# Kernel tuning notes

Hardware: AMD Instinct MI355X
Metric: run time of the kernel (lower is better)

## Reference

```python
import jax, jax.numpy as jnp
import numpy as np
from jax import lax

# module hyperparams (from init_kwargs)
K = 7
STRIDE = 1
PAD = 3
DIL = 1


def setup_inputs() -> dict:
    key = jax.random.key(0)
    ks = jax.random.split(key, 5)
    B, Cin, Cout, L = 4, 256, 256, 8192
    x = jax.random.normal(ks[0], (B, Cin, L), jnp.float32)
    # main conv weight (Cout, Cin, K), kaiming-ish scale
    weight = jax.random.normal(ks[1], (Cout, Cin, K), jnp.float32) * (1.0 / np.sqrt(Cin * K))
    bias = jax.random.normal(ks[2], (Cout,), jnp.float32) * 0.01
    # offset conv: Conv1d(Cin -> K, kernel K); small values so sampling is perturbed but in-range
    offset_w = jax.random.normal(ks[3], (K, Cin, K), jnp.float32) * 0.01
    offset_b = jax.random.normal(ks[4], (K,), jnp.float32) * 0.01
    return {"x": x, "weight": weight, "bias": bias, "offset_w": offset_w, "offset_b": offset_b}


def reference(x, weight, bias, offset_w, offset_b):
    B, Cin, L = x.shape
    out_len = (L + 2 * PAD - DIL * (K - 1) - 1) // STRIDE + 1

    # offset conv: (B, Cin, L) -> (B, K, out_len)
    offsets = lax.conv_general_dilated(
        x, offset_w, window_strides=(STRIDE,), padding=[(PAD, PAD)],
        rhs_dilation=(DIL,), dimension_numbers=("NCH", "OIH", "NCH"))
    offsets = offsets + offset_b[None, :, None]
    offsets = jnp.transpose(offsets, (0, 2, 1))  # (B, out_len, K)

    # standard sampling locations (1, out_len, K), shifted by padding as in original
    p = jnp.arange(out_len, dtype=jnp.float32)[None, :, None] * STRIDE
    p_k = (jnp.arange(K, dtype=jnp.float32) - (K - 1) / 2.0) * DIL
    loc = p + p_k[None, None, :] + PAD + offsets  # (B, out_len, K)

    # linear interpolation (clamped endpoints, matching torch clamp order)
    x0 = jnp.floor(loc).astype(jnp.int32)
    x1 = x0 + 1
    x0c = jnp.clip(x0, 0, L - 1)
    x1c = jnp.clip(x1, 0, L - 1)
    wa = x1c.astype(jnp.float32) - loc  # weights use clamped indices, as original
    wb = loc - x0c.astype(jnp.float32)

    # gather: per batch, (Cin, L)[:, (out_len, K)] -> (Cin, out_len, K)
    gather = jax.vmap(lambda xb, ib: xb[:, ib])
    fa = gather(x, x0c)  # (B, Cin, out_len, K)
    fb = gather(x, x1c)
    interp = wa[:, None] * fa + wb[:, None] * fb  # (B, Cin, out_len, K)

    # einsum 'blki,oik->blo' with interp laid out as (B, i=Cin, l, k)
    out = jnp.einsum("bilk,oik->bol", interp, weight) + bias[None, :, None]
    return out
```

## Files before the change

kernel.cpp:

```cpp
#include <hip/hip_runtime.h>
#include <hip/hip_bf16.h>


#define B_    4
#define CIN   256
#define COUT  256
#define LEN   8192
#define KK    7
#define NTOT  (B_ * LEN)
#define QTOT  (CIN * KK)
#define LPITCH 232

typedef short s16x8 __attribute__((ext_vector_type(8)));
typedef int   s32x4 __attribute__((ext_vector_type(4)));
typedef float f32x4 __attribute__((ext_vector_type(4)));

static __device__ __forceinline__ unsigned f2bf(float f) {
  union { float f; unsigned u; } u; u.f = f;
  unsigned r = u.u + 0x7FFF + ((u.u >> 16) & 1);
  return r >> 16;
}

static __device__ __forceinline__ int cvt_pk_bf16(float a, float b) {
  int r;
  asm("v_cvt_pk_bf16_f32 %0, %1, %2" : "=v"(r) : "v"(a), "v"(b));
  return r;
}

__global__ __launch_bounds__(256) void loc_partial(
    const float* __restrict__ X, const float* __restrict__ OW,
    float* __restrict__ Partial) {
  __shared__ float red[4][256][KK];

  const int t    = threadIdx.x;
  const int lane = t & 63;
  const int wu   = __builtin_amdgcn_readfirstlane(t >> 6);
  const int cg   = blockIdx.x >> 7;
  const int nb   = (blockIdx.x & 127) << 8;
  const int b    = nb >> 13;
  const int l0   = nb & (LEN - 1);

  float acc[KK][4];
#pragma unroll
  for (int k = 0; k < KK; ++k)
#pragma unroll
    for (int r = 0; r < 4; ++r) acc[k][r] = 0.0f;

#pragma unroll 2
  for (int ii = 0; ii < 16; ++ii) {
    const int i = cg * 64 + wu * 16 + ii;
    float owv[49];
#pragma unroll
    for (int k = 0; k < KK; ++k)
#pragma unroll
      for (int j = 0; j < KK; ++j)
        owv[k * 7 + j] = OW[(k * CIN + i) * KK + j];

    const float* xr = X + ((size_t)(b * CIN + i) << 13);
#pragma unroll
    for (int r = 0; r < 4; ++r) {
      const int lr = l0 + lane + 64 * r;
      float xv[KK];
#pragma unroll
      for (int j = 0; j < KK; ++j) {
        int pos = lr + j - 3;
        xv[j] = ((unsigned)pos < LEN) ? xr[pos] : 0.0f;
      }
#pragma unroll
      for (int k = 0; k < KK; ++k)
#pragma unroll
        for (int j = 0; j < KK; ++j)
          acc[k][r] += xv[j] * owv[k * 7 + j];
    }
  }

#pragma unroll
  for (int k = 0; k < KK; ++k)
#pragma unroll
    for (int r = 0; r < 4; ++r) red[wu][lane + 64 * r][k] = acc[k][r];
  __syncthreads();

#pragma unroll
  for (int k = 0; k < KK; ++k) {
    float s = red[0][t][k] + red[1][t][k] + red[2][t][k] + red[3][t][k];
    Partial[((size_t)(cg * 7 + k) << 15) + nb + t] = s;
  }
}

__global__ __launch_bounds__(256) void loc_reduce(
    const float* __restrict__ Partial, const float* __restrict__ OB,
    float* __restrict__ Loc) {
  int n = blockIdx.x * 256 + threadIdx.x;
  int l = n & (LEN - 1);
#pragma unroll
  for (int k = 0; k < KK; ++k) {
    float s = (float)(l + k) + OB[k];
#pragma unroll
    for (int cg = 0; cg < 4; ++cg)
      s += Partial[((size_t)(cg * 7 + k) << 15) + n];
    Loc[((size_t)k << 15) + n] = s;
  }
}

__global__ __launch_bounds__(256) void wt_build(
    const float* __restrict__ W, unsigned short* __restrict__ Wf) {
  __shared__ float Wl[16 * 32 * KK];
  const int t  = threadIdx.x;
  const int ot = blockIdx.x >> 3;
  const int c  = blockIdx.x & 7;

  for (int e = t; e < 16 * 32 * KK; e += 256) {
    int o = e / 224;
    int r = e - o * 224;
    Wl[e] = W[(size_t)(ot * 16 + o) * QTOT + c * 224 + r];
  }
  __syncthreads();

  const int lane = t & 63;
  const int sg   = t >> 6;
  const int ol   = lane & 15;
  const int ig   = lane >> 4;
  for (int s = sg; s < KK; s += 4) {
    s16x8 v;
#pragma unroll
    for (int j = 0; j < 8; ++j)
      v[j] = (short)f2bf(Wl[ol * 224 + (ig * 8 + j) * KK + s]);
    int f = (ot * 8 + c) * KK + s;
    *(s16x8*)(Wf + ((size_t)f << 9) + (lane << 3)) = v;
  }
}

__global__ __launch_bounds__(512, 4) void main_kernel(
    const float* __restrict__ X, const unsigned short* __restrict__ Wf,
    const float* __restrict__ Bias, const float* __restrict__ Loc,
    float* __restrict__ Out) {
  __shared__ unsigned short Il[2][64][LPITCH];

  const int t    = threadIdx.x;
  const int lane = t & 63;
  const int w    = t >> 6;
  const int n0   = blockIdx.x << 6;
  const int b    = n0 >> 13;
  const float* Xb = X + ((size_t)b << 21);

  const bool stager = (t < 448);
  const int nl = t & 63;
  const int kt = t >> 6;

  float c0 = 0.f, c1 = 0.f;
  const float* xp = Xb;
  if (stager) {
    float locv = Loc[((size_t)kt << 15) + n0 + nl];
    int x0  = (int)floorf(locv);
    int x0c = min(max(x0, 0), LEN - 1);
    int x1c = min(max(x0 + 1, 0), LEN - 1);
    float wa = (float)x1c - locv;
    float wb = locv - (float)x0c;
    bool hi = (x0 >= LEN - 1);
    bool lo = (x0 < 0);
    c0 = (hi ? 0.f : wa) + (lo ? wb : 0.f);
    c1 = (hi ? wa : 0.f) + (lo ? 0.f : wb);
    xp = Xb + min(max(x0, 0), LEN - 2);
  }

  f32x4 acc[2][4];
#pragma unroll
  for (int a = 0; a < 2; ++a)
#pragma unroll
    for (int cc = 0; cc < 4; ++cc) acc[a][cc] = (f32x4){0.f, 0.f, 0.f, 0.f};

  const int mrow = lane & 15;
  const int quad = lane >> 4;

  float f0[16], f1[16];

#define GATHER_H(chunk, h)                                        \
  if (stager) {                                                   \
    _Pragma("unroll")                                             \
    for (int m = 0; m < 16; ++m) {                                \
      const float* xr = xp + ((size_t)((chunk) * 32 + (h) * 16 + m) << 13); \
      f0[m] = xr[0];                                              \
      f1[m] = xr[1];                                              \
    }                                                             \
  }

#define CVT_H(dst, h)                                             \
  if (stager) {                                                   \
    s32x4 v0, v1;                                                 \
    _Pragma("unroll")                                             \
    for (int m = 0; m < 4; ++m) {                                 \
      float a = c0 * f0[2 * m]     + c1 * f1[2 * m];              \
      float d = c0 * f0[2 * m + 1] + c1 * f1[2 * m + 1];          \
      v0[m] = cvt_pk_bf16(a, d);                                  \
    }                                                             \
    _Pragma("unroll")                                             \
    for (int m = 0; m < 4; ++m) {                                 \
      float a = c0 * f0[8 + 2 * m]     + c1 * f1[8 + 2 * m];      \
      float d = c0 * f0[8 + 2 * m + 1] + c1 * f1[8 + 2 * m + 1];  \
      v1[m] = cvt_pk_bf16(a, d);                                  \
    }                                                             \
    *(s32x4*)((dst) + nl * LPITCH + kt * 32 + (h) * 16)     = v0; \
    *(s32x4*)((dst) + nl * LPITCH + kt * 32 + (h) * 16 + 8) = v1; \
  }

#define AFL(ttv, sv)                                              \
  (*(const s16x8*)(Wf + ((size_t)(((w * 2 + (ttv)) * 8 + c) * KK + (sv)) << 9) + (lane << 3)))

#define MSTEP(sv, a0, a1) {                                                        \
    const s16x8 b0 = *(const s16x8*)(Icur + (mrow)      * LPITCH + (sv) * 32 + quad * 8); \
    const s16x8 b1 = *(const s16x8*)(Icur + (16 + mrow) * LPITCH + (sv) * 32 + quad * 8); \
    acc[0][0] = __builtin_amdgcn_mfma_f32_16x16x32_bf16(a0, b0, acc[0][0], 0, 0, 0); \
    acc[1][0] = __builtin_amdgcn_mfma_f32_16x16x32_bf16(a1, b0, acc[1][0], 0, 0, 0); \
    acc[0][1] = __builtin_amdgcn_mfma_f32_16x16x32_bf16(a0, b1, acc[0][1], 0, 0, 0); \
    acc[1][1] = __builtin_amdgcn_mfma_f32_16x16x32_bf16(a1, b1, acc[1][1], 0, 0, 0); \
    const s16x8 b2 = *(const s16x8*)(Icur + (32 + mrow) * LPITCH + (sv) * 32 + quad * 8); \
    const s16x8 b3 = *(const s16x8*)(Icur + (48 + mrow) * LPITCH + (sv) * 32 + quad * 8); \
    acc[0][2] = __builtin_amdgcn_mfma_f32_16x16x32_bf16(a0, b2, acc[0][2], 0, 0, 0); \
    acc[1][2] = __builtin_amdgcn_mfma_f32_16x16x32_bf16(a1, b2, acc[1][2], 0, 0, 0); \
    acc[0][3] = __builtin_amdgcn_mfma_f32_16x16x32_bf16(a0, b3, acc[0][3], 0, 0, 0); \
    acc[1][3] = __builtin_amdgcn_mfma_f32_16x16x32_bf16(a1, b3, acc[1][3], 0, 0, 0); \
  }

  {
    unsigned short* I0 = &Il[0][0][0];
    GATHER_H(0, 0) CVT_H(I0, 0)
    GATHER_H(0, 1) CVT_H(I0, 1)
  }
  __syncthreads();

  for (int c = 0; c < 8; ++c) {
    const int cur = c & 1;
    const unsigned short* Icur = &Il[cur][0][0];
    unsigned short*       Inxt = &Il[cur ^ 1][0][0];

    s16x8 afA[2][4];
#pragma unroll
    for (int tt = 0; tt < 2; ++tt)
#pragma unroll
      for (int s = 0; s < 4; ++s) afA[tt][s] = AFL(tt, s);
    __builtin_amdgcn_sched_barrier(0);

    if (c < 7) { GATHER_H(c + 1, 0) }
    __builtin_amdgcn_sched_barrier(0);

    MSTEP(0, afA[0][0], afA[1][0])

    s16x8 afB[2][3];
#pragma unroll
    for (int tt = 0; tt < 2; ++tt)
#pragma unroll
      for (int s = 0; s < 3; ++s) afB[tt][s] = AFL(tt, 4 + s);
    __builtin_amdgcn_sched_barrier(0);

    MSTEP(1, afA[0][1], afA[1][1])

    if (c < 7) { CVT_H(Inxt, 0) GATHER_H(c + 1, 1) }
    __builtin_amdgcn_sched_barrier(0);

    MSTEP(2, afA[0][2], afA[1][2])
    MSTEP(3, afA[0][3], afA[1][3])
    MSTEP(4, afB[0][0], afB[1][0])

    if (c < 7) { CVT_H(Inxt, 1) }

    MSTEP(5, afB[0][1], afB[1][1])
    MSTEP(6, afB[0][2], afB[1][2])
    if (c < 7) __syncthreads();
  }
#undef GATHER_H
#undef CVT_H
#undef AFL
#undef MSTEP

  const int lbase = (n0 & (LEN - 1)) + mrow;
#pragma unroll
  for (int tt = 0; tt < 2; ++tt) {
    const int obase = (w * 2 + tt) * 16 + quad * 4;
#pragma unroll
    for (int r = 0; r < 4; ++r) {
      const int o = obase + r;
      const float bv = Bias[o];
      float* orow = Out + (((size_t)(b * COUT + o)) << 13) + lbase;
#pragma unroll
      for (int nt = 0; nt < 4; ++nt)
        orow[nt * 16] = acc[tt][nt][r] + bv;
    }
  }
}

extern "C" void kernel_launch(void* const* d_in, const int* in_sizes, int n_in,
                              void* d_out, int out_size, void* d_ws, size_t ws_size,
                              hipStream_t stream) {
  const float* X    = (const float*)d_in[0];
  const float* W    = (const float*)d_in[1];
  const float* Bias = (const float*)d_in[2];
  const float* OW   = (const float*)d_in[3];
  const float* OB   = (const float*)d_in[4];
  float* Out = (float*)d_out;

  float* Loc = (float*)d_ws;
  unsigned short* Wf = (unsigned short*)(Loc + (size_t)NTOT * KK);
  float* Partial = (float*)(Wf + (size_t)COUT * QTOT);

  loc_partial<<<4 * 128, 256, 0, stream>>>(X, OW, Partial);
  loc_reduce<<<NTOT / 256, 256, 0, stream>>>(Partial, OB, Loc);
  wt_build<<<128, 256, 0, stream>>>(W, Wf);
  main_kernel<<<NTOT / 64, 512, 0, stream>>>(X, Wf, Bias, Loc, Out);
}
```

Before: 184.7 us.

## Warp-specialize main kernel into MFMA waves and gather/stager waves

Splits the 8 waves of each block into 4 compute waves that each own 64 output channels (4x4 MFMA tiles) and 4 staging waves that gather, interpolate and convert X into the double-buffered LDS tile. Previously all waves interleaved gathering with MFMA under manual sched_barriers. The intent is to overlap global gather latency with matrix math through role separation and to simplify scheduling. In exchange, compute waves hold twice the accumulators and now load weight fragments inline instead of prefetching them. Half the waves do no MFMA, which may reduce matrix throughput or occupancy under the 512x4 launch bounds.

```diff
diff --git a/kernel.cpp b/kernel.cpp
--- a/kernel.cpp
+++ b/kernel.cpp
@@ -138,152 +138,165 @@
 
   const int t    = threadIdx.x;
   const int lane = t & 63;
-  const int w    = t >> 6;
+  const int w    = __builtin_amdgcn_readfirstlane(t >> 6);
   const int n0   = blockIdx.x << 6;
   const int b    = n0 >> 13;
   const float* Xb = X + ((size_t)b << 21);
 
-  const bool stager = (t < 448);
-  const int nl = t & 63;
-  const int kt = t >> 6;
-
-  float c0 = 0.f, c1 = 0.f;
-  const float* xp = Xb;
-  if (stager) {
-    float locv = Loc[((size_t)kt << 15) + n0 + nl];
-    int x0  = (int)floorf(locv);
-    int x0c = min(max(x0, 0), LEN - 1);
-    int x1c = min(max(x0 + 1, 0), LEN - 1);
-    float wa = (float)x1c - locv;
-    float wb = locv - (float)x0c;
-    bool hi = (x0 >= LEN - 1);
-    bool lo = (x0 < 0);
-    c0 = (hi ? 0.f : wa) + (lo ? wb : 0.f);
-    c1 = (hi ? wa : 0.f) + (lo ? 0.f : wb);
-    xp = Xb + min(max(x0, 0), LEN - 2);
-  }
-
-  f32x4 acc[2][4];
-#pragma unroll
-  for (int a = 0; a < 2; ++a)
-#pragma unroll
-    for (int cc = 0; cc < 4; ++cc) acc[a][cc] = (f32x4){0.f, 0.f, 0.f, 0.f};
-
   const int mrow = lane & 15;
   const int quad = lane >> 4;
-
-  float f0[16], f1[16];
-
-#define GATHER_H(chunk, h)                                        \
-  if (stager) {                                                   \
-    _Pragma("unroll")                                             \
-    for (int m = 0; m < 16; ++m) {                                \
-      const float* xr = xp + ((size_t)((chunk) * 32 + (h) * 16 + m) << 13); \
-      f0[m] = xr[0];                                              \
-      f1[m] = xr[1];                                              \
-    }                                                             \
-  }
-
-#define CVT_H(dst, h)                                             \
-  if (stager) {                                                   \
-    s32x4 v0, v1;                                                 \
-    _Pragma("unroll")                                             \
-    for (int m = 0; m < 4; ++m) {                                 \
-      float a = c0 * f0[2 * m]     + c1 * f1[2 * m];              \
-      float d = c0 * f0[2 * m + 1] + c1 * f1[2 * m + 1];          \
-      v0[m] = cvt_pk_bf16(a, d);                                  \
-    }                                                             \
-    _Pragma("unroll")                                             \
-    for (int m = 0; m < 4; ++m) {                                 \
-      float a = c0 * f0[8 + 2 * m]     + c1 * f1[8 + 2 * m];      \
-      float d = c0 * f0[8 + 2 * m + 1] + c1 * f1[8 + 2 * m + 1];  \
-      v1[m] = cvt_pk_bf16(a, d);                                  \
-    }                                                             \
-    *(s32x4*)((dst) + nl * LPITCH + kt * 32 + (h) * 16)     = v0; \
-    *(s32x4*)((dst) + nl * LPITCH + kt * 32 + (h) * 16 + 8) = v1; \
-  }
-
-#define AFL(ttv, sv)                                              \
-  (*(const s16x8*)(Wf + ((size_t)(((w * 2 + (ttv)) * 8 + c) * KK + (sv)) << 9) + (lane << 3)))
-
-#define MSTEP(sv, a0, a1) {                                                        \
-    const s16x8 b0 = *(const s16x8*)(Icur + (mrow)      * LPITCH + (sv) * 32 + quad * 8); \
-    const s16x8 b1 = *(const s16x8*)(Icur + (16 + mrow) * LPITCH + (sv) * 32 + quad * 8); \
+  const bool mf  = (w < 4);
+
+  const int sw   = w - 4;
+  const int nl   = lane;
+  const int ktA  = sw;
+  const int ktB  = sw + 4;
+  const bool hasB = (!mf) && (ktB < KK);
+
+  float c0A = 0.f, c1A = 0.f, c0B = 0.f, c1B = 0.f;
+  int offA = 0, offB = 0;
+  if (!mf) {
+    {
+      float locv = Loc[((size_t)ktA << 15) + n0 + nl];
+      int x0  = (int)floorf(locv);
+      int x0c = min(max(x0, 0), LEN - 1);
+      int x1c = min(max(x0 + 1, 0), LEN - 1);
+      float wa = (float)x1c - locv;
+      float wb = locv - (float)x0c;
+      bool hi = (x0 >= LEN - 1), lo = (x0 < 0);
+      c0A = (hi ? 0.f : wa) + (lo ? wb : 0.f);
+      c1A = (hi ? wa : 0.f) + (lo ? 0.f : wb);
+      offA = min(max(x0, 0), LEN - 2);
+    }
+    if (hasB) {
+      float locv = Loc[((size_t)ktB << 15) + n0 + nl];
+      int x0  = (int)floorf(locv);
+      int x0c = min(max(x0, 0), LEN - 1);
+      int x1c = min(max(x0 + 1, 0), LEN - 1);
+      float wa = (float)x1c - locv;
+      float wb = locv - (float)x0c;
+      bool hi = (x0 >= LEN - 1), lo = (x0 < 0);
+      c0B = (hi ? 0.f : wa) + (lo ? wb : 0.f);
+      c1B = (hi ? wa : 0.f) + (lo ? 0.f : wb);
+      offB = min(max(x0, 0), LEN - 2);
+    }
+  }
+
+  f32x4 acc[4][4];
+  if (mf) {
+#pragma unroll
+    for (int a = 0; a < 4; ++a)
+#pragma unroll
+      for (int cc = 0; cc < 4; ++cc) acc[a][cc] = (f32x4){0.f, 0.f, 0.f, 0.f};
+  }
+
+  float fX0[8], fX1[8], fY0[8], fY1[8];
+
+#define GQ(j, F0, F1) {                                               \
+    const int st_ = (j) >> 2; const int hh_ = (j) & 3;                \
+    if (st_ == 0 || hasB) {                                           \
+      const int o_ = st_ ? offBc : offAc;                             \
+      _Pragma("unroll")                                               \
+      for (int m = 0; m < 8; ++m) {                                   \
+        const int idx = o_ + ((hh_ * 8 + m) << 13);                   \
+        F0[m] = Xb[idx];                                              \
+        F1[m] = Xb[idx + 1];                                          \
+      }                                                               \
+    } }
+
+#define CQ(j, F0, F1, DST) {                                          \
+    const int st_ = (j) >> 2; const int hh_ = (j) & 3;                \
+    if (st_ == 0 || hasB) {                                           \
+      const float c0_ = st_ ? c0B : c0A;                              \
+      const float c1_ = st_ ? c1B : c1A;                              \
+      const int   kt_ = st_ ? ktB : ktA;                              \
+      s32x4 vv;                                                       \
+      _Pragma("unroll")                                               \
+      for (int m = 0; m < 4; ++m) {                                   \
+        float a = c0_ * F0[2 * m]     + c1_ * F1[2 * m];              \
+        float d = c0_ * F0[2 * m + 1] + c1_ * F1[2 * m + 1];          \
+        vv[m] = cvt_pk_bf16(a, d);                                    \
+      }                                                               \
+      *(s32x4*)((DST) + nl * LPITCH + kt_ * 32 + hh_ * 8) = vv;       \
+    } }
+
+#define STAGE(DST, CH0) {                                             \
+    const int offAc = offA + ((CH0) << 13);                           \
+    const int offBc = offB + ((CH0) << 13);                           \
+    GQ(0, fX0, fX1) GQ(1, fY0, fY1)                                   \
+    CQ(0, fX0, fX1, DST) GQ(2, fX0, fX1)                              \
+    CQ(1, fY0, fY1, DST) GQ(3, fY0, fY1)                              \
+    CQ(2, fX0, fX1, DST) GQ(4, fX0, fX1)                              \
+    CQ(3, fY0, fY1, DST) GQ(5, fY0, fY1)                              \
+    CQ(4, fX0, fX1, DST) GQ(6, fX0, fX1)                              \
+    CQ(5, fY0, fY1, DST) GQ(7, fY0, fY1)                              \
+    CQ(6, fX0, fX1, DST)                                              \
+    CQ(7, fY0, fY1, DST)                                              \
+  }
+
+#define AFL(ttv, sv)                                                  \
+  (*(const s16x8*)(Wf + ((size_t)(((w * 4 + (ttv)) * 8 + c) * KK + (sv)) << 9) + (lane << 3)))
+
+#define BLD(ro, sv)                                                   \
+  (*(const s16x8*)(Icur + ((ro) + mrow) * LPITCH + (sv) * 32 + quad * 8))
+
+#define MSTEP4(sv) {                                                  \
+    const s16x8 a0 = AFL(0, sv), a1 = AFL(1, sv);                     \
+    const s16x8 a2 = AFL(2, sv), a3 = AFL(3, sv);                     \
+    const s16x8 b0 = BLD(0, sv), b1 = BLD(16, sv);                    \
     acc[0][0] = __builtin_amdgcn_mfma_f32_16x16x32_bf16(a0, b0, acc[0][0], 0, 0, 0); \
     acc[1][0] = __builtin_amdgcn_mfma_f32_16x16x32_bf16(a1, b0, acc[1][0], 0, 0, 0); \
+    acc[2][0] = __builtin_amdgcn_mfma_f32_16x16x32_bf16(a2, b0, acc[2][0], 0, 0, 0); \
+    acc[3][0] = __builtin_amdgcn_mfma_f32_16x16x32_bf16(a3, b0, acc[3][0], 0, 0, 0); \
     acc[0][1] = __builtin_amdgcn_mfma_f32_16x16x32_bf16(a0, b1, acc[0][1], 0, 0, 0); \
     acc[1][1] = __builtin_amdgcn_mfma_f32_16x16x32_bf16(a1, b1, acc[1][1], 0, 0, 0); \
-    const s16x8 b2 = *(const s16x8*)(Icur + (32 + mrow) * LPITCH + (sv) * 32 + quad * 8); \
-    const s16x8 b3 = *(const s16x8*)(Icur + (48 + mrow) * LPITCH + (sv) * 32 + quad * 8); \
+    acc[2][1] = __builtin_amdgcn_mfma_f32_16x16x32_bf16(a2, b1, acc[2][1], 0, 0, 0); \
+    acc[3][1] = __builtin_amdgcn_mfma_f32_16x16x32_bf16(a3, b1, acc[3][1], 0, 0, 0); \
+    const s16x8 b2 = BLD(32, sv), b3 = BLD(48, sv);                   \
     acc[0][2] = __builtin_amdgcn_mfma_f32_16x16x32_bf16(a0, b2, acc[0][2], 0, 0, 0); \
     acc[1][2] = __builtin_amdgcn_mfma_f32_16x16x32_bf16(a1, b2, acc[1][2], 0, 0, 0); \
+    acc[2][2] = __builtin_amdgcn_mfma_f32_16x16x32_bf16(a2, b2, acc[2][2], 0, 0, 0); \
+    acc[3][2] = __builtin_amdgcn_mfma_f32_16x16x32_bf16(a3, b2, acc[3][2], 0, 0, 0); \
     acc[0][3] = __builtin_amdgcn_mfma_f32_16x16x32_bf16(a0, b3, acc[0][3], 0, 0, 0); \
     acc[1][3] = __builtin_amdgcn_mfma_f32_16x16x32_bf16(a1, b3, acc[1][3], 0, 0, 0); \
-  }
-
-  {
-    unsigned short* I0 = &Il[0][0][0];
-    GATHER_H(0, 0) CVT_H(I0, 0)
-    GATHER_H(0, 1) CVT_H(I0, 1)
-  }
+    acc[2][3] = __builtin_amdgcn_mfma_f32_16x16x32_bf16(a2, b3, acc[2][3], 0, 0, 0); \
+    acc[3][3] = __builtin_amdgcn_mfma_f32_16x16x32_bf16(a3, b3, acc[3][3], 0, 0, 0); \
+  }
+
+  if (!mf) { STAGE(&Il[0][0][0], 0) }
   __syncthreads();
 
   for (int c = 0; c < 8; ++c) {
-    const int cur = c & 1;
-    const unsigned short* Icur = &Il[cur][0][0];
-    unsigned short*       Inxt = &Il[cur ^ 1][0][0];
-
-    s16x8 afA[2][4];
-#pragma unroll
-    for (int tt = 0; tt < 2; ++tt)
-#pragma unroll
-      for (int s = 0; s < 4; ++s) afA[tt][s] = AFL(tt, s);
-    __builtin_amdgcn_sched_barrier(0);
-
-    if (c < 7) { GATHER_H(c + 1, 0) }
-    __builtin_amdgcn_sched_barrier(0);
-
-    MSTEP(0, afA[0][0], afA[1][0])
-
-    s16x8 afB[2][3];
-#pragma unroll
-    for (int tt = 0; tt < 2; ++tt)
-#pragma unroll
-      for (int s = 0; s < 3; ++s) afB[tt][s] = AFL(tt, 4 + s);
-    __builtin_amdgcn_sched_barrier(0);
-
-    MSTEP(1, afA[0][1], afA[1][1])
-
-    if (c < 7) { CVT_H(Inxt, 0) GATHER_H(c + 1, 1) }
-    __builtin_amdgcn_sched_barrier(0);
-
-    MSTEP(2, afA[0][2], afA[1][2])
-    MSTEP(3, afA[0][3], afA[1][3])
-    MSTEP(4, afB[0][0], afB[1][0])
-
-    if (c < 7) { CVT_H(Inxt, 1) }
-
-    MSTEP(5, afB[0][1], afB[1][1])
-    MSTEP(6, afB[0][2], afB[1][2])
-    if (c < 7) __syncthreads();
-  }
-#undef GATHER_H
-#undef CVT_H
+    if (mf) {
+      const unsigned short* Icur = &Il[c & 1][0][0];
+      MSTEP4(0) MSTEP4(1) MSTEP4(2) MSTEP4(3) MSTEP4(4) MSTEP4(5) MSTEP4(6)
+    } else if (c < 7) {
+      unsigned short* Inxt = &Il[(c & 1) ^ 1][0][0];
+      STAGE(Inxt, (c + 1) * 32)
+    }
+    __syncthreads();
+  }
+#undef GQ
+#undef CQ
+#undef STAGE
 #undef AFL
-#undef MSTEP
-
-  const int lbase = (n0 & (LEN - 1)) + mrow;
-#pragma unroll
-  for (int tt = 0; tt < 2; ++tt) {
-    const int obase = (w * 2 + tt) * 16 + quad * 4;
-#pragma unroll
-    for (int r = 0; r < 4; ++r) {
-      const int o = obase + r;
-      const float bv = Bias[o];
-      float* orow = Out + (((size_t)(b * COUT + o)) << 13) + lbase;
-#pragma unroll
-      for (int nt = 0; nt < 4; ++nt)
-        orow[nt * 16] = acc[tt][nt][r] + bv;
+#undef BLD
+#undef MSTEP4
+
+  if (mf) {
+    const int lbase = (n0 & (LEN - 1)) + mrow;
+#pragma unroll
+    for (int tt = 0; tt < 4; ++tt) {
+      const int obase = (w * 4 + tt) * 16 + quad * 4;
+#pragma unroll
+      for (int r = 0; r < 4; ++r) {
+        const int o = obase + r;
+        const float bv = Bias[o];
+        float* orow = Out + (((size_t)(b * COUT + o)) << 13) + lbase;
+#pragma unroll
+        for (int nt = 0; nt < 4; ++nt)
+          orow[nt * 16] = acc[tt][nt][r] + bv;
+      }
     }
   }
 }
```

New measurement: 246.3 us. 33.4% more time.
